# Kernel optimization log

Measured on AMD Instinct MI355X. Metric: run time of the kernel, lower is better.

Reference implementation:

```python
import jax, jax.numpy as jnp
import numpy as np

B, M, D, OUT = 16384, 4096, 512, 128


def setup_inputs() -> dict:
    key = jax.random.key(0)
    ks = jax.random.split(key, 5)
    x = jax.random.normal(ks[0], (B, D), dtype=jnp.float32)
    support = jax.random.normal(ks[1], (M, D), dtype=jnp.float32)
    gamma = jnp.float32(1.0)
    head_w = jax.random.normal(ks[2], (OUT, M), dtype=jnp.float32) / np.sqrt(M)
    head_b = jax.random.normal(ks[3], (OUT,), dtype=jnp.float32) * 0.01
    scale = jnp.ones((1,), dtype=jnp.float32)
    shift = jnp.zeros((1,), dtype=jnp.float32)
    return {"x": x, "support": support, "gamma": gamma,
            "head_w": head_w, "head_b": head_b,
            "scale": scale, "shift": shift}


def reference(x, support, gamma, head_w, head_b, scale, shift):
    x2 = jnp.sum(x * x, axis=-1, keepdims=True)           # [B, 1]
    s2 = jnp.sum(support * support, axis=-1)              # [M]
    xs = jnp.einsum('bd,md->bm', x, support)              # [B, M]
    sqdist = jnp.maximum(x2 + s2[None, :] - 2.0 * xs, 0.0)
    k = jnp.exp(-gamma * sqdist)                          # RBF kernel [B, M]
    out = jnp.einsum('bm,om->bo', k, head_w) + head_b     # linear head [B, OUT]
    return scale * out + shift
```

## Files before the change

kernel.cpp:

```cpp
#include <hip/hip_runtime.h>

typedef unsigned int u32;
typedef unsigned short u16;
typedef unsigned char u8;
typedef __attribute__((ext_vector_type(8))) __bf16 bf16x8;
typedef __attribute__((ext_vector_type(4))) float f32x4;
typedef __attribute__((ext_vector_type(4))) int i32x4;

#define NB 16384
#define NM 4096
#define ND 512
#define NOUT 128
#define L2E 1.44269504088896340736f


#define WAITLG(N) do { asm volatile("s_waitcnt vmcnt(" #N ") lgkmcnt(0)" ::: "memory"); \
                       __builtin_amdgcn_sched_barrier(0); } while (0)
#define SB0() __builtin_amdgcn_sched_barrier(0)

__device__ __forceinline__ u16 f2bf(float f) {
  u32 u = __float_as_uint(f);
  u += 0x7FFFu + ((u >> 16) & 1u);
  return (u16)(u >> 16);
}

__device__ __forceinline__ u8 f2fp8(float f) {
  u32 u = __float_as_uint(f);
  u32 s = (u >> 24) & 0x80u;
  u32 au = u & 0x7FFFFFFFu;
  if (au < 0x3C800000u) return (u8)s;
  au += 0x000FFFFFu + ((au >> 20) & 1u);
  u32 e = (au >> 23) - 120u;
  u32 m = (au >> 20) & 7u;
  return (u8)(s | (e << 3) | m);
}

__device__ __forceinline__ void stage16(const void* g, void* l) {
  __builtin_amdgcn_global_load_lds((__attribute__((address_space(1))) void*)g,
                                   (__attribute__((address_space(3))) void*)l,
                                   16, 0, 0);
}

__device__ __forceinline__ bf16x8 ldg_b128(const void* p) {
  i32x4 r;
  asm volatile("global_load_dwordx4 %0, %1, off" : "=&v"(r) : "v"(p) : "memory");
  return __builtin_bit_cast(bf16x8, r);
}

__device__ __forceinline__ uint4 pack8bf(float4 v0, float4 v1) {
  uint4 pk;
  pk.x = (u32)f2bf(v0.x) | ((u32)f2bf(v0.y) << 16);
  pk.y = (u32)f2bf(v0.z) | ((u32)f2bf(v0.w) << 16);
  pk.z = (u32)f2bf(v1.x) | ((u32)f2bf(v1.y) << 16);
  pk.w = (u32)f2bf(v1.z) | ((u32)f2bf(v1.w) << 16);
  return pk;
}

__device__ __forceinline__ uint2 pack8f8(float4 v0, float4 v1) {
  uint2 pk;
  pk.x = (u32)f2fp8(v0.x) | ((u32)f2fp8(v0.y) << 8) |
         ((u32)f2fp8(v0.z) << 16) | ((u32)f2fp8(v0.w) << 24);
  pk.y = (u32)f2fp8(v1.x) | ((u32)f2fp8(v1.y) << 8) |
         ((u32)f2fp8(v1.z) << 16) | ((u32)f2fp8(v1.w) << 24);
  return pk;
}

__global__ __launch_bounds__(256) void prep_all(const float* __restrict__ x,
                                                const float* __restrict__ s,
                                                const float* __restrict__ hw,
                                                const float* __restrict__ gamma_p,
                                                u8*  __restrict__ x_ws,
                                                u8*  __restrict__ s_ws,
                                                u16* __restrict__ hw_ws,
                                                float* __restrict__ x2g,
                                                float* __restrict__ s2g,
                                                float* __restrict__ out) {
  __shared__ uint2 t8[2048];
  __shared__ uint4 t16[2048];
  const int tid = threadIdx.x, bid = blockIdx.x;
  const int lane = tid & 63, w = tid >> 6;

  if (bid < 640) {
    const bool isx = bid < 512;
    const int blk = isx ? bid : (bid - 512);
    const float* src_m = isx ? x : s;
    u8*    dst_ws = isx ? x_ws : s_ws;
    float* sq_out = isx ? x2g : s2g;
    const float gl   = gamma_p[0] * L2E;
    const float cmul = isx ? 1.0f : (-2.0f * gl);
    const int big  = isx ? (blk >> 1) : (blk >> 2);
    const int roff = isx ? ((blk & 1) * 32) : ((blk & 3) * 32);
    const int rows = isx ? 64 : 128;

    #pragma unroll
    for (int p = 0; p < 8; ++p) {
      const int row = p * 4 + w;
      const float* src = src_m + (size_t)(blk * 32 + row) * ND + lane * 8;
      float4 v0 = *(const float4*)src;
      float4 v1 = *(const float4*)(src + 4);
      float ss = v0.x*v0.x + v0.y*v0.y + v0.z*v0.z + v0.w*v0.w
               + v1.x*v1.x + v1.y*v1.y + v1.z*v1.z + v1.w*v1.w;
      #pragma unroll
      for (int off = 32; off > 0; off >>= 1) ss += __shfl_down(ss, off);
      if (lane == 0) sq_out[blk * 32 + row] = gl * ss;
      v0.x *= cmul; v0.y *= cmul; v0.z *= cmul; v0.w *= cmul;
      v1.x *= cmul; v1.y *= cmul; v1.z *= cmul; v1.w *= cmul;
      t8[lane * 32 + ((row + lane) & 31)] = pack8f8(v0, v1);
    }
    __syncthreads();
    #pragma unroll
    for (int p = 0; p < 8; ++p) {
      const int kg = p * 8 + (tid >> 5);
      const int row = tid & 31;
      uint2 pk = t8[kg * 32 + ((row + kg) & 31)];
      *(uint2*)&dst_ws[(((size_t)(big * 64 + kg)) * rows + roff + row) * 8] = pk;
    }
  } else if (bid < 672) {
    const int blk = bid - 640;
    #pragma unroll
    for (int p = 0; p < 8; ++p) {
      const int o = p * 16 + (tid >> 4);
      const int kg = tid & 15;
      const float* src = hw + (size_t)o * NM + blk * 128 + kg * 8;
      float4 v0 = *(const float4*)src;
      float4 v1 = *(const float4*)(src + 4);
      t16[o * 16 + ((kg + o) & 15)] = pack8bf(v0, v1);
    }
    __syncthreads();
    #pragma unroll
    for (int it = 0; it < 8; ++it) {
      const int kg = it * 2 + (tid >> 7);
      const int o = tid & 127;
      uint4 pk = t16[o * 16 + ((kg + o) & 15)];
      *(uint4*)&hw_ws[(((size_t)(blk * 16 + kg)) * 128 + o) * 8] = pk;
    }
  } else {
    float4* o4 = (float4*)out;
    const float4 z = {0.f, 0.f, 0.f, 0.f};
    size_t base = (size_t)(bid - 672) * 8192 + tid;
    #pragma unroll 8
    for (int i = 0; i < 32; ++i) o4[base + (size_t)i * 256] = z;
  }
}

__global__ __launch_bounds__(512, 2)
void rbf_fused(const u8* __restrict__ x_ws, const u8* __restrict__ s_ws,
               const u16* __restrict__ hw_ws, const float* __restrict__ x2g,
               const float* __restrict__ s2g, const float* __restrict__ head_b,
               const float* __restrict__ scale_p, const float* __restrict__ shift_p,
               float* __restrict__ out)
{
  extern __shared__ __align__(16) char smem[];

  const int tid  = threadIdx.x;
  const int w    = tid >> 6;
  const int lane = tid & 63;
  const int quad = lane >> 4;
  const int l16  = lane & 15;
  const int wr   = w & 3;
  const int wc   = w >> 2;
  const int xcd  = blockIdx.x & 7;
  const int rb   = (blockIdx.x >> 3) * 2 + (xcd & 1);
  const int half = xcd >> 1;
  const int b0   = rb * 64;

  const float vscale = scale_p[0];
  const float vshift = shift_p[0];

  const u8* xsrc = x_ws + (size_t)rb * 32768;
  const u8* ssrc = s_ws + (size_t)(half * 8) * 65536;

  auto stage_grp = [&](int mt_s, int grp_s) {
    const u8* sp = ssrc + (size_t)mt_s * 65536 + grp_s * 8192;
    stage16(sp + tid * 16, smem + 32768 + (grp_s & 3) * 8192 + tid * 16);
  };

  #pragma unroll
  for (int i = 0; i < 4; ++i)
    stage16(xsrc + i * 8192 + tid * 16, smem + i * 8192 + tid * 16);
  SB0();
  f32x4 x2v = *(const f32x4*)&x2g[b0 + wr * 16 + quad * 4];
  SB0();
  stage_grp(0, 0); SB0();
  stage_grp(0, 1); SB0();
  stage_grp(0, 2);
  asm volatile("s_waitcnt vmcnt(2)" ::: "memory");
  SB0();
  __builtin_amdgcn_s_barrier();
  SB0();

  const f32x4 zf = {0.f, 0.f, 0.f, 0.f};
  f32x4 acc_xs[4], acc_out[4];
  #pragma unroll
  for (int c = 0; c < 4; ++c) { acc_xs[c] = zf; acc_out[c] = zf; }

  bf16x8 b2[4];

  #pragma unroll 1
  for (int mt = 0; mt < 8; ++mt) {
    const int mtg = half * 8 + mt;
    float s2v[4];

    #pragma unroll
    for (int grp = 0; grp < 8; ++grp) {
      long long a[2], bf[2][4];
      #pragma unroll
      for (int k2 = 0; k2 < 2; ++k2) {
        const int kc = grp * 2 + k2;
        a[k2] = *(const long long*)(smem + ((kc * 4 + quad) * 64 + wr * 16 + l16) * 8);
        #pragma unroll
        for (int c = 0; c < 4; ++c)
          bf[k2][c] = *(const long long*)(smem + 32768 + (grp & 3) * 8192 +
                                          ((k2 * 4 + quad) * 128 + wc * 64 + c * 16 + l16) * 8);
      }
      bf16x8 a2;
      if (mt > 0 && (grp & 1) == 0) {
        const int kg = (grp >> 1) * 4 + quad;
        a2 = *(const bf16x8*)(smem + 65536 + kg * 1024 + (wr * 16 + l16) * 16);
      }
      if (grp == 0) {
        #pragma unroll
        for (int c = 0; c < 4; ++c)
          s2v[c] = s2g[mtg * 128 + wc * 64 + c * 16 + l16];
      }
      if ((grp & 1) == 1 && !(mt == 7 && grp == 7)) {
        int ks, sm;
        if (grp < 7) { ks = (grp + 1) >> 1; sm = mtg - 1; }
        else         { ks = 0;              sm = mtg;     }
        if (sm < 0) sm = 0;
        const int kg = ks * 4 + quad;
        const size_t sb = (size_t)(sm * 16 + kg);
        #pragma unroll
        for (int c = 0; c < 4; ++c)
          b2[c] = ldg_b128(hw_ws + (sb * 128 + wc * 64 + c * 16 + l16) * 8);
      }

      SB0();

      if (grp <= 4)     stage_grp(mt, grp + 3);
      else if (mt < 7)  stage_grp(mt + 1, grp - 5);

      if (grp == 0)              WAITLG(6);
      else if ((grp & 1) == 0)   { if (mt < 7 || grp < 6) WAITLG(2); else WAITLG(0); }
      else if (grp == 7)         { if (mt < 7) WAITLG(7); else WAITLG(0); }
      else                       WAITLG(7);

      __builtin_amdgcn_s_barrier();
      SB0();

      __builtin_amdgcn_s_setprio(1);
      #pragma unroll
      for (int k2 = 0; k2 < 2; ++k2)
        #pragma unroll
        for (int c = 0; c < 4; ++c)
          acc_xs[c] = __builtin_amdgcn_mfma_f32_16x16x32_fp8_fp8(a[k2], bf[k2][c],
                                                                 acc_xs[c], 0, 0, 0);
      if (mt > 0 && (grp & 1) == 0) {
        #pragma unroll
        for (int c = 0; c < 4; ++c)
          acc_out[c] = __builtin_amdgcn_mfma_f32_16x16x32_bf16(a2, b2[c], acc_out[c], 0, 0, 0);
      }
      __builtin_amdgcn_s_setprio(0);
    }

    #pragma unroll
    for (int c = 0; c < 4; ++c) {
      const int cl = wc * 64 + c * 16 + l16;
      char* kbase = smem + 65536 + (cl >> 3) * 1024 + (cl & 7) * 2;
      #pragma unroll
      for (int i = 0; i < 4; ++i) {
        const int row = wr * 16 + quad * 4 + i;
        const float t = acc_xs[c][i] + x2v[i] + s2v[c];
        float kv = __builtin_amdgcn_exp2f(-t);
        kv = fminf(kv, 1.0f);
        *(u16*)(kbase + row * 16) = (u16)(__float_as_uint(kv) >> 16);
        acc_xs[c][i] = 0.0f;
      }
    }
    asm volatile("s_waitcnt lgkmcnt(0)" ::: "memory");
    SB0();
    __builtin_amdgcn_s_barrier();
    SB0();
  }

  #pragma unroll
  for (int ks = 0; ks < 4; ++ks) {
    const int kg = ks * 4 + quad;
    const size_t sb = (size_t)((half * 8 + 7) * 16 + kg);
    bf16x8 bb[4];
    #pragma unroll
    for (int c = 0; c < 4; ++c)
      bb[c] = *(const bf16x8*)(hw_ws + (sb * 128 + wc * 64 + c * 16 + l16) * 8);
    bf16x8 a2 = *(const bf16x8*)(smem + 65536 + kg * 1024 + (wr * 16 + l16) * 16);
    #pragma unroll
    for (int c = 0; c < 4; ++c)
      acc_out[c] = __builtin_amdgcn_mfma_f32_16x16x32_bf16(a2, bb[c], acc_out[c], 0, 0, 0);
  }

  float addv[4];
  #pragma unroll
  for (int c = 0; c < 4; ++c) {
    const int col = wc * 64 + c * 16 + l16;
    addv[c] = (half == 0) ? (vscale * head_b[col] + vshift) : 0.0f;
  }
  #pragma unroll
  for (int c = 0; c < 4; ++c) {
    const int col = wc * 64 + c * 16 + l16;
    #pragma unroll
    for (int i = 0; i < 4; ++i) {
      const int row = b0 + wr * 16 + quad * 4 + i;
      atomicAdd(&out[(size_t)row * NOUT + col], vscale * acc_out[c][i] + addv[c]);
    }
  }
}

extern "C" void kernel_launch(void* const* d_in, const int* in_sizes, int n_in,
                              void* d_out, int out_size, void* d_ws, size_t ws_size,
                              hipStream_t stream) {
  const float* x       = (const float*)d_in[0];
  const float* support = (const float*)d_in[1];
  const float* gamma   = (const float*)d_in[2];
  const float* head_w  = (const float*)d_in[3];
  const float* head_b  = (const float*)d_in[4];
  const float* scale   = (const float*)d_in[5];
  const float* shift   = (const float*)d_in[6];
  float* out = (float*)d_out;

  char* w = (char*)d_ws;
  u8*    x_ws  = (u8*)(w);
  u8*    s_ws  = (u8*)(w + 8388608);
  u16*   hw_ws = (u16*)(w + 10485760);
  float* x2g   = (float*)(w + 11534336);
  float* s2g   = (float*)(w + 11599872);

  static bool lds_init = false;
  if (!lds_init) {
    hipFuncSetAttribute(reinterpret_cast<const void*>(rbf_fused),
                        hipFuncAttributeMaxDynamicSharedMemorySize, 81920);
    lds_init = true;
  }

  prep_all<<<736, 256, 0, stream>>>(x, support, head_w, gamma,
                                    x_ws, s_ws, hw_ws, x2g, s2g, out);
  rbf_fused<<<1024, 512, 81920, stream>>>(x_ws, s_ws, hw_ws, x2g, s2g,
                                          head_b, scale, shift, out);
}
```

Measured before the change: 212.2 us.

## Halve block row tile to 32 rows with 256 threads and double-buffered staging

Shrinks each fused block from 64 rows / 512 threads to 32 rows / 256 threads, doubling grid size and targeting four blocks per CU with 40 KB static LDS. The support-tile staging changes from a 4-deep ring with fine-grained vmcnt waits to a simple two-buffer ping-pong with a full wait and barrier each group. This is meant to raise occupancy and let more independent blocks hide latency. In exchange, each block reloads the support tiles for half as many rows, which doubles support traffic through L2, and the stricter per-step barriers reduce overlap within a block.

```diff
diff --git a/kernel.cpp b/kernel.cpp
--- a/kernel.cpp
+++ b/kernel.cpp
@@ -16,6 +16,8 @@
 
 #define WAITLG(N) do { asm volatile("s_waitcnt vmcnt(" #N ") lgkmcnt(0)" ::: "memory"); \
                        __builtin_amdgcn_sched_barrier(0); } while (0)
+#define LGKM(N) do { asm volatile("s_waitcnt lgkmcnt(" #N ")" ::: "memory"); \
+                     __builtin_amdgcn_sched_barrier(0); } while (0)
 #define SB0() __builtin_amdgcn_sched_barrier(0)
 
 __device__ __forceinline__ u16 f2bf(float f) {
@@ -143,49 +145,51 @@
   }
 }
 
-__global__ __launch_bounds__(512, 2)
+__global__ __launch_bounds__(256, 4)
 void rbf_fused(const u8* __restrict__ x_ws, const u8* __restrict__ s_ws,
                const u16* __restrict__ hw_ws, const float* __restrict__ x2g,
                const float* __restrict__ s2g, const float* __restrict__ head_b,
                const float* __restrict__ scale_p, const float* __restrict__ shift_p,
                float* __restrict__ out)
 {
-  extern __shared__ __align__(16) char smem[];
+  __shared__ __align__(16) char smem[40960];
 
   const int tid  = threadIdx.x;
   const int w    = tid >> 6;
   const int lane = tid & 63;
   const int quad = lane >> 4;
   const int l16  = lane & 15;
-  const int wr   = w & 3;
-  const int wc   = w >> 2;
+  const int wr   = w & 1;
+  const int wc   = w >> 1;
   const int xcd  = blockIdx.x & 7;
   const int rb   = (blockIdx.x >> 3) * 2 + (xcd & 1);
   const int half = xcd >> 1;
-  const int b0   = rb * 64;
+  const int b0   = rb * 32;
 
   const float vscale = scale_p[0];
   const float vshift = shift_p[0];
 
-  const u8* xsrc = x_ws + (size_t)rb * 32768;
+  const u8* xsrc = x_ws + (size_t)(rb >> 1) * 32768;
+  const int roff = (rb & 1) * 256;
   const u8* ssrc = s_ws + (size_t)(half * 8) * 65536;
 
-  auto stage_grp = [&](int mt_s, int grp_s) {
+  auto stage_tile = [&](int mt_s, int grp_s, int buf) {
     const u8* sp = ssrc + (size_t)mt_s * 65536 + grp_s * 8192;
-    stage16(sp + tid * 16, smem + 32768 + (grp_s & 3) * 8192 + tid * 16);
+    char* dp = smem + 16384 + buf * 8192;
+    stage16(sp + tid * 16, dp + tid * 16);
+    stage16(sp + 4096 + tid * 16, dp + 4096 + tid * 16);
   };
 
-  #pragma unroll
-  for (int i = 0; i < 4; ++i)
-    stage16(xsrc + i * 8192 + tid * 16, smem + i * 8192 + tid * 16);
-  SB0();
   f32x4 x2v = *(const f32x4*)&x2g[b0 + wr * 16 + quad * 4];
   SB0();
-  stage_grp(0, 0); SB0();
-  stage_grp(0, 1); SB0();
-  stage_grp(0, 2);
-  asm volatile("s_waitcnt vmcnt(2)" ::: "memory");
+  #pragma unroll
+  for (int i = 0; i < 4; ++i) {
+    const u8* src = xsrc + (size_t)(i * 16 + (tid >> 4)) * 512 + roff + (tid & 15) * 16;
+    stage16(src, smem + i * 4096 + tid * 16);
+  }
   SB0();
+  stage_tile(0, 0, 0);
+  WAITLG(0);
   __builtin_amdgcn_s_barrier();
   SB0();
 
@@ -203,70 +207,68 @@
 
     #pragma unroll
     for (int grp = 0; grp < 8; ++grp) {
-      long long a[2], bf[2][4];
+      const int buf = grp & 1;
+
+      if (grp == 0) {
+        #pragma unroll
+        for (int c = 0; c < 4; ++c)
+          s2v[c] = s2g[mtg * 128 + wc * 64 + c * 16 + l16];
+        SB0();
+      }
+      if (!(mt == 7 && grp == 7)) {
+        if (grp < 7) stage_tile(mt, grp + 1, buf ^ 1);
+        else         stage_tile(mt + 1, 0, buf ^ 1);
+      }
+      SB0();
+      if ((grp & 1) == 1 && ((grp < 7) ? (mt >= 1) : (mt <= 6))) {
+        const int ks = (grp < 7) ? ((grp + 1) >> 1) : 0;
+        const int sm = (grp < 7) ? (mtg - 1) : mtg;
+        const size_t sb = (size_t)(sm * 16 + ks * 4 + quad);
+        #pragma unroll
+        for (int c = 0; c < 4; ++c)
+          b2[c] = ldg_b128(hw_ws + (sb * 128 + wc * 64 + c * 16 + l16) * 8);
+      }
+      SB0();
+
+      long long aF[2], bF[2][4];
       #pragma unroll
       for (int k2 = 0; k2 < 2; ++k2) {
         const int kc = grp * 2 + k2;
-        a[k2] = *(const long long*)(smem + ((kc * 4 + quad) * 64 + wr * 16 + l16) * 8);
-        #pragma unroll
-        for (int c = 0; c < 4; ++c)
-          bf[k2][c] = *(const long long*)(smem + 32768 + (grp & 3) * 8192 +
-                                          ((k2 * 4 + quad) * 128 + wc * 64 + c * 16 + l16) * 8);
+        aF[k2] = *(const long long*)(smem + ((kc * 4 + quad) * 32 + wr * 16 + l16) * 8);
+        #pragma unroll
+        for (int c = 0; c < 4; ++c)
+          bF[k2][c] = *(const long long*)(smem + 16384 + buf * 8192 +
+                        ((k2 * 4 + quad) * 128 + wc * 64 + c * 16 + l16) * 8);
       }
       bf16x8 a2;
-      if (mt > 0 && (grp & 1) == 0) {
-        const int kg = (grp >> 1) * 4 + quad;
-        a2 = *(const bf16x8*)(smem + 65536 + kg * 1024 + (wr * 16 + l16) * 16);
-      }
-      if (grp == 0) {
-        #pragma unroll
-        for (int c = 0; c < 4; ++c)
-          s2v[c] = s2g[mtg * 128 + wc * 64 + c * 16 + l16];
-      }
-      if ((grp & 1) == 1 && !(mt == 7 && grp == 7)) {
-        int ks, sm;
-        if (grp < 7) { ks = (grp + 1) >> 1; sm = mtg - 1; }
-        else         { ks = 0;              sm = mtg;     }
-        if (sm < 0) sm = 0;
-        const int kg = ks * 4 + quad;
-        const size_t sb = (size_t)(sm * 16 + kg);
-        #pragma unroll
-        for (int c = 0; c < 4; ++c)
-          b2[c] = ldg_b128(hw_ws + (sb * 128 + wc * 64 + c * 16 + l16) * 8);
-      }
-
-      SB0();
-
-      if (grp <= 4)     stage_grp(mt, grp + 3);
-      else if (mt < 7)  stage_grp(mt + 1, grp - 5);
-
-      if (grp == 0)              WAITLG(6);
-      else if ((grp & 1) == 0)   { if (mt < 7 || grp < 6) WAITLG(2); else WAITLG(0); }
-      else if (grp == 7)         { if (mt < 7) WAITLG(7); else WAITLG(0); }
-      else                       WAITLG(7);
-
-      __builtin_amdgcn_s_barrier();
-      SB0();
+      if (mt > 0 && (grp & 1) == 0)
+        a2 = *(const bf16x8*)(smem + 32768 + ((grp >> 1) * 4 + quad) * 512 +
+                              (wr * 16 + l16) * 16);
+      LGKM(0);
 
       __builtin_amdgcn_s_setprio(1);
       #pragma unroll
       for (int k2 = 0; k2 < 2; ++k2)
         #pragma unroll
         for (int c = 0; c < 4; ++c)
-          acc_xs[c] = __builtin_amdgcn_mfma_f32_16x16x32_fp8_fp8(a[k2], bf[k2][c],
-                                                                 acc_xs[c], 0, 0, 0);
+          acc_xs[c] = __builtin_amdgcn_mfma_f32_16x16x32_fp8_fp8(
+              aF[k2], bF[k2][c], acc_xs[c], 0, 0, 0);
       if (mt > 0 && (grp & 1) == 0) {
         #pragma unroll
         for (int c = 0; c < 4; ++c)
           acc_out[c] = __builtin_amdgcn_mfma_f32_16x16x32_bf16(a2, b2[c], acc_out[c], 0, 0, 0);
       }
       __builtin_amdgcn_s_setprio(0);
+
+      WAITLG(0);
+      __builtin_amdgcn_s_barrier();
+      SB0();
     }
 
     #pragma unroll
     for (int c = 0; c < 4; ++c) {
       const int cl = wc * 64 + c * 16 + l16;
-      char* kbase = smem + 65536 + (cl >> 3) * 1024 + (cl & 7) * 2;
+      char* kbase = smem + 32768 + (cl >> 3) * 512 + (cl & 7) * 2;
       #pragma unroll
       for (int i = 0; i < 4; ++i) {
         const int row = wr * 16 + quad * 4 + i;
@@ -277,24 +279,23 @@
         acc_xs[c][i] = 0.0f;
       }
     }
-    asm volatile("s_waitcnt lgkmcnt(0)" ::: "memory");
-    SB0();
+    LGKM(0);
     __builtin_amdgcn_s_barrier();
     SB0();
   }
 
   #pragma unroll
   for (int ks = 0; ks < 4; ++ks) {
-    const int kg = ks * 4 + quad;
-    const size_t sb = (size_t)((half * 8 + 7) * 16 + kg);
+    const size_t sb = (size_t)((half * 8 + 7) * 16 + ks * 4 + quad);
     bf16x8 bb[4];
     #pragma unroll
     for (int c = 0; c < 4; ++c)
       bb[c] = *(const bf16x8*)(hw_ws + (sb * 128 + wc * 64 + c * 16 + l16) * 8);
-    bf16x8 a2 = *(const bf16x8*)(smem + 65536 + kg * 1024 + (wr * 16 + l16) * 16);
+    bf16x8 aa = *(const bf16x8*)(smem + 32768 + (ks * 4 + quad) * 512 +
+                                 (wr * 16 + l16) * 16);
     #pragma unroll
     for (int c = 0; c < 4; ++c)
-      acc_out[c] = __builtin_amdgcn_mfma_f32_16x16x32_bf16(a2, bb[c], acc_out[c], 0, 0, 0);
+      acc_out[c] = __builtin_amdgcn_mfma_f32_16x16x32_bf16(aa, bb[c], acc_out[c], 0, 0, 0);
   }
 
   float addv[4];
@@ -333,15 +334,8 @@
   float* x2g   = (float*)(w + 11534336);
   float* s2g   = (float*)(w + 11599872);
 
-  static bool lds_init = false;
-  if (!lds_init) {
-    hipFuncSetAttribute(reinterpret_cast<const void*>(rbf_fused),
-                        hipFuncAttributeMaxDynamicSharedMemorySize, 81920);
-    lds_init = true;
-  }
-
   prep_all<<<736, 256, 0, stream>>>(x, support, head_w, gamma,
                                     x_ws, s_ws, hw_ws, x2g, s2g, out);
-  rbf_fused<<<1024, 512, 81920, stream>>>(x_ws, s_ws, hw_ws, x2g, s2g,
-                                          head_b, scale, shift, out);
-}
+  rbf_fused<<<2048, 256, 0, stream>>>(x_ws, s_ws, hw_ws, x2g, s2g,
+                                      head_b, scale, shift, out);
+}
```

Result: faster. 187.5 us (-11.6%).
